# Kernel optimization log

Hardware: AMD Instinct MI355X
Metric: run time of the kernel (lower is better)

Reference implementation:

```python
import jax, jax.numpy as jnp
import numpy as np

BATCH, SEQ, HIDDEN = 2, 4096, 4096
HEADS, HEAD_DIM, BLOCK = 32, 128, 256
LAYER_IDX, N_LAYERS = 1, 32
EPS = 1e-5


def setup_inputs() -> dict:
    key = jax.random.key(0)
    ks = jax.random.split(key, 5)
    s = 0.02
    return {
        "hidden_states": jax.random.normal(ks[0], (BATCH, SEQ, HIDDEN), jnp.float32),
        "qkv_w": jax.random.normal(ks[1], (3 * HEADS * HEAD_DIM, HIDDEN), jnp.float32) * s,
        "out_w": jax.random.normal(ks[2], (HIDDEN, HEADS * HEAD_DIM), jnp.float32) * s,
        "gate_w": jax.random.normal(ks[3], (HEADS * HEAD_DIM, HIDDEN), jnp.float32) * s,
        "norm_w": jnp.ones((HEADS * HEAD_DIM,), jnp.float32),
    }


def _decays():
    # slope_rate: (h,1,1)
    base = 1.0 / 2.0 ** (8.0 / HEADS)
    exponent = jnp.arange(HEADS, dtype=jnp.float32) + 1.0
    factor = 1.0 - LAYER_IDX / (N_LAYERS - 1 + 1e-5) + 1e-5
    slope = (base ** exponent * factor)[:, None, None]
    r = jnp.arange(BLOCK, dtype=jnp.float32) + 1.0
    q_decay = jnp.exp(-slope * r[:, None])                 # (h, block, 1)
    k_decay = jnp.exp(-slope * (BLOCK - r)[:, None])       # (h, block, 1)
    diff = r[:, None] - r[None, :]                         # (block, block): i - j
    diag = slope[None] * diff[None, None]                  # (1, h, block, block)
    diag = jnp.where(diag >= 0, -diag, -jnp.inf)
    diag_decay = jnp.exp(diag)                             # causal intra-block decay
    block_decay = jnp.exp(-slope * BLOCK)                  # (h,1,1)
    return q_decay, k_decay, diag_decay, block_decay


def reference(hidden_states, qkv_w, out_w, gate_w, norm_w):
    b, s, _ = hidden_states.shape
    h, d, bs = HEADS, HEAD_DIM, BLOCK
    nb = s // bs
    q_decay, k_decay, diag_decay, block_decay = _decays()

    # qkv projection + silu, split per-head into q,k,v
    qkv = jax.nn.silu(hidden_states @ qkv_w.T)             # (b,s,3hd)
    qkv = qkv.reshape(b, s, h, 3, d)
    q = jnp.moveaxis(qkv[:, :, :, 0], 2, 1)                # (b,h,s,d)
    k = jnp.moveaxis(qkv[:, :, :, 1], 2, 1)
    v = jnp.moveaxis(qkv[:, :, :, 2], 2, 1)

    # split sequence into blocks, scan leading axis = block index
    def to_blocks(x):
        return jnp.moveaxis(x.reshape(b, h, nb, bs, d), 2, 0)  # (nb,b,h,bs,d)

    qb, kb, vb = to_blocks(q), to_blocks(k), to_blocks(v)

    def step(kv, blk):
        cq, ck, cv = blk
        # intra-block quadratic attention with causal decay
        scores = jnp.einsum('bhnd,bhmd->bhnm', cq, ck) * diag_decay
        intra = jnp.einsum('bhnm,bhmd->bhnd', scores, cv)
        # inter-block via decayed recurrent state kv: (b,h,d,d)
        inter = jnp.einsum('bhnd,bhde->bhne', cq * q_decay, kv)
        kv_next = kv * block_decay + jnp.einsum('bhnd,bhne->bhde', ck * k_decay, cv)
        return kv_next, intra + inter

    kv0 = jnp.zeros((b, h, d, d), hidden_states.dtype)
    _, out_blocks = jax.lax.scan(step, kv0, (qb, kb, vb))  # (nb,b,h,bs,d)

    attn = jnp.moveaxis(out_blocks, 0, 2)                  # (b,h,nb,bs,d)
    attn = attn.reshape(b, h, s, d).transpose(0, 2, 1, 3).reshape(b, s, h * d)

    # RMSNorm (fp32 accumulation, as MixtralRMSNorm)
    xf = attn.astype(jnp.float32)
    xf = xf * jax.lax.rsqrt(jnp.mean(xf * xf, axis=-1, keepdims=True) + EPS)
    normed = norm_w * xf.astype(attn.dtype)

    gate = jax.nn.sigmoid(hidden_states @ gate_w.T)
    return (gate * normed) @ out_w.T
```

## Files before the change

kernel.cpp:

```cpp
#include <hip/hip_runtime.h>

typedef unsigned short u16;
typedef __attribute__((ext_vector_type(4))) float f32x4;
typedef __attribute__((ext_vector_type(8))) __bf16 bf16x8;

#define SEQ   4096
#define HID   4096
#define HID3  12288

__device__ __forceinline__ float bf2f(u16 u){
  union { unsigned int i; float f; } v; v.i = ((unsigned int)u) << 16; return v.f;
}
__device__ __forceinline__ u16 f2bf(float f){
  union { float f; unsigned int i; } v; v.f = f;
  unsigned int r = (v.i + 0x7FFFu + ((v.i >> 16) & 1u)) >> 16;
  return (u16)r;
}
__device__ __forceinline__ float slope_of(int h){
  const float factor = 1.0f - 1.0f/(31.0f + 1e-5f) + 1e-5f;
  return exp2f(-0.25f * (float)(h + 1)) * factor;
}
__device__ __forceinline__ bf16x8 ld_bf8(const u16* p){
  return __builtin_bit_cast(bf16x8, *(const uint4*)p);
}
__device__ __forceinline__ void gload_lds16(const u16* g, u16* l){
  __builtin_amdgcn_global_load_lds((const __attribute__((address_space(1))) void*)g,
                                   (__attribute__((address_space(3))) void*)l, 16, 0, 0);
}

__global__ __launch_bounds__(256) void cvt_kernel(const float* __restrict__ in,
                                                  u16* __restrict__ out, long n){
  long i = ((long)blockIdx.x * 256 + threadIdx.x) * 4;
  long stride = (long)gridDim.x * 1024;
  for (; i < n; i += stride){
    float4 v = *(const float4*)(in + i);
    ushort4 o;
    o.x = f2bf(v.x); o.y = f2bf(v.y); o.z = f2bf(v.z); o.w = f2bf(v.w);
    *(ushort4*)(out + i) = o;
  }
}

template<int EPI>
__global__ __launch_bounds__(512) void gemm256(
    const u16* __restrict__ A, const u16* __restrict__ B, void* __restrict__ C,
    const u16* __restrict__ Aux, int M, int N, int K)
{
  __shared__ u16 ring[5][16384];
  const int t = threadIdx.x;
  const int w = t >> 6, l = t & 63, lr = l & 15, lk = l >> 4;
  const int mw = w >> 2, nw = w & 3;
  const int nbn = N >> 8;
  int nwg = gridDim.x;
  int bid = blockIdx.x;
  int bswz = (bid & 7) * (nwg >> 3) + (bid >> 3);
  int bm = bswz / nbn, bn = bswz % nbn;
  const u16* Abase = A + (long)(bm * 256) * K;
  const u16* Bbase = B + (long)(bn * 256) * K;
  const int NT = K >> 6;

  int sr[2], sku[2];
#pragma unroll
  for (int i = 0; i < 2; ++i){
    int dr = i * 64 + (t >> 3);
    int ul = (t & 7) ^ (dr & 7);
    sr[i]  = 2 * dr + (ul >> 2);
    sku[i] = ul & 3;
  }
  int offA[8], offB[4];
#pragma unroll
  for (int fn = 0; fn < 8; ++fn){
    int row = mw * 128 + fn * 16 + lr;
    offA[fn] = (row >> 1) * 64 + (((((row & 1) << 2) + lk) ^ ((row >> 1) & 7)) << 3);
  }
#pragma unroll
  for (int fe = 0; fe < 4; ++fe){
    int row = nw * 64 + fe * 16 + lr;
    offB[fe] = (row >> 1) * 64 + (((((row & 1) << 2) + lk) ^ ((row >> 1) & 7)) << 3);
  }

  auto stageA = [&](int kt, int c, int slot, int i){
    gload_lds16(Abase + (long)sr[i] * K + kt * 64 + c * 32 + sku[i] * 8,
                &ring[slot][i * 4096 + w * 512]);
  };
  auto stageB = [&](int kt, int c, int slot, int i){
    gload_lds16(Bbase + (long)sr[i] * K + kt * 64 + c * 32 + sku[i] * 8,
                &ring[slot][8192 + i * 4096 + w * 512]);
  };

  f32x4 acc[8][4] = {};

  stageA(0,0,0,0); stageA(0,0,0,1); stageB(0,0,0,0); stageB(0,0,0,1);
  stageA(0,1,1,0); stageA(0,1,1,1); stageB(0,1,1,0); stageB(0,1,1,1);
  if (1 < NT){ stageA(1,0,2,0); stageA(1,0,2,1); stageB(1,0,2,0); stageB(1,0,2,1); }
  asm volatile("s_waitcnt vmcnt(4)" ::: "memory");
  __builtin_amdgcn_s_barrier();

  int sa = 0;
  for (int p = 0; p < NT; ++p){
    int sb = sa + 1; if (sb >= 5) sb -= 5;
    int sx = sa + 3; if (sx >= 5) sx -= 5;
    int sy = sa + 4; if (sy >= 5) sy -= 5;
    const u16* Aa = &ring[sa][0];
    const u16* Ab = &ring[sb][0];
    const u16* Ba = &ring[sa][8192];
    const u16* Bb = &ring[sb][8192];
    bf16x8 bh[4][2], af[4][2][2];
#pragma unroll
    for (int q = 0; q < 4; ++q){
      if (q == 0){
#pragma unroll
        for (int fe = 0; fe < 4; ++fe){
          bh[fe][0] = ld_bf8(Ba + offB[fe]);
          bh[fe][1] = ld_bf8(Bb + offB[fe]);
        }
#pragma unroll
        for (int fnl = 0; fnl < 2; ++fnl){
          af[0][fnl][0] = ld_bf8(Aa + offA[fnl]);
          af[0][fnl][1] = ld_bf8(Ab + offA[fnl]);
        }
#pragma unroll
        for (int fnl = 0; fnl < 2; ++fnl){
          af[1][fnl][0] = ld_bf8(Aa + offA[2 + fnl]);
          af[1][fnl][1] = ld_bf8(Ab + offA[2 + fnl]);
        }
        if (p + 1 < NT){ stageA(p+1, 1, sx, 0); stageA(p+1, 1, sx, 1); }
      } else if (q == 1){
#pragma unroll
        for (int fnl = 0; fnl < 2; ++fnl){
          af[2][fnl][0] = ld_bf8(Aa + offA[4 + fnl]);
          af[2][fnl][1] = ld_bf8(Ab + offA[4 + fnl]);
        }
        if (p + 1 < NT){ stageB(p+1, 1, sx, 0); stageB(p+1, 1, sx, 1); }
      } else if (q == 2){
#pragma unroll
        for (int fnl = 0; fnl < 2; ++fnl){
          af[3][fnl][0] = ld_bf8(Aa + offA[6 + fnl]);
          af[3][fnl][1] = ld_bf8(Ab + offA[6 + fnl]);
        }
        if (p + 2 < NT){ stageA(p+2, 0, sy, 0); stageA(p+2, 0, sy, 1); }
      } else {
        if (p + 2 < NT){ stageB(p+2, 0, sy, 0); stageB(p+2, 0, sy, 1); }
      }
      if (q < 3) asm volatile("s_waitcnt lgkmcnt(4)" ::: "memory");
      else       asm volatile("s_waitcnt lgkmcnt(0)" ::: "memory");
      __builtin_amdgcn_sched_barrier(0);
      __builtin_amdgcn_s_setprio(1);
#pragma unroll
      for (int fnl = 0; fnl < 2; ++fnl)
#pragma unroll
        for (int fe = 0; fe < 4; ++fe){
          acc[q*2+fnl][fe] = __builtin_amdgcn_mfma_f32_16x16x32_bf16(af[q][fnl][0], bh[fe][0], acc[q*2+fnl][fe], 0, 0, 0);
          acc[q*2+fnl][fe] = __builtin_amdgcn_mfma_f32_16x16x32_bf16(af[q][fnl][1], bh[fe][1], acc[q*2+fnl][fe], 0, 0, 0);
        }
      __builtin_amdgcn_s_setprio(0);
    }
    if (p + 2 < NT) asm volatile("s_waitcnt vmcnt(4)" ::: "memory");
    else            asm volatile("s_waitcnt vmcnt(0)" ::: "memory");
    __builtin_amdgcn_s_barrier();
    sa += 2; if (sa >= 5) sa -= 5;
  }

  long crow = (long)bm * 256 + mw * 128 + lk * 4;
  long ccol = (long)bn * 256 + nw * 64 + lr;
#pragma unroll
  for (int fn = 0; fn < 8; ++fn)
#pragma unroll
    for (int fe = 0; fe < 4; ++fe)
#pragma unroll
      for (int reg = 0; reg < 4; ++reg){
        long row = crow + fn * 16 + reg;
        long col = ccol + fe * 16;
        float x = acc[fn][fe][reg];
        if (EPI == 0){
          ((u16*)C)[row * N + col] = f2bf(x / (1.0f + __expf(-x)));
        } else if (EPI == 1){
          float g = 1.0f / (1.0f + __expf(-x));
          ((u16*)C)[row * N + col] = f2bf(g * bf2f(Aux[row * N + col]));
        } else {
          ((float*)C)[row * N + col] = x;
        }
      }
}

__global__ __launch_bounds__(256) void attn_contrib(
    const u16* __restrict__ qkv, float* __restrict__ ct)
{
  __shared__ u16 kb[256 * 128];
  __shared__ u16 vb[256 * 128];
  __shared__ float kdec[256];
  int wg = blockIdx.x;
  int bh = wg >> 4, blk = wg & 15;
  int b = bh >> 5, h = bh & 31;
  int t = threadIdx.x;
  float slope = slope_of(h);
  kdec[t] = __expf(-slope * (float)(255 - t));
  const u16* kg = qkv + ((long)(b * SEQ + blk * 256)) * HID3 + h * 384 + 128;
  const u16* vg = kg + 128;
#pragma unroll
  for (int i = 0; i < 16; ++i){
    int chunk = t + i * 256;
    int row = chunk >> 4, c8 = (chunk & 15) << 3;
    *(uint4*)&kb[row * 128 + c8] = *(const uint4*)&kg[(long)row * HID3 + c8];
    *(uint4*)&vb[row * 128 + c8] = *(const uint4*)&vg[(long)row * HID3 + c8];
  }
  __syncthreads();
  int e0 = (t >> 4) << 3, d0 = (t & 15) << 3;
  float acc[8][8];
#pragma unroll
  for (int i = 0; i < 8; ++i)
#pragma unroll
    for (int j = 0; j < 8; ++j) acc[i][j] = 0.f;
  for (int n = 0; n < 256; ++n){
    float kd = kdec[n];
    uint4 vv = *(const uint4*)&vb[n * 128 + e0];
    uint4 kk = *(const uint4*)&kb[n * 128 + d0];
    const u16* vs = (const u16*)&vv;
    const u16* ks = (const u16*)&kk;
    float ve[8], kf[8];
#pragma unroll
    for (int x = 0; x < 8; ++x){ ve[x] = bf2f(vs[x]); kf[x] = bf2f(ks[x]) * kd; }
#pragma unroll
    for (int i = 0; i < 8; ++i)
#pragma unroll
      for (int j = 0; j < 8; ++j) acc[i][j] += ve[i] * kf[j];
  }
  float* out = ct + (long)wg * 16384;
#pragma unroll
  for (int i = 0; i < 8; ++i){
    *(float4*)&out[(e0 + i) * 128 + d0]     = make_float4(acc[i][0], acc[i][1], acc[i][2], acc[i][3]);
    *(float4*)&out[(e0 + i) * 128 + d0 + 4] = make_float4(acc[i][4], acc[i][5], acc[i][6], acc[i][7]);
  }
}

__global__ __launch_bounds__(256) void attn_scan(const float* __restrict__ ct,
                                                 u16* __restrict__ stTb)
{
  int g = blockIdx.x;
  int bh = g >> 2, sl = g & 3;
  int t = threadIdx.x;
  float bdec = __expf(-slope_of(bh & 31) * 256.0f);
  float cur[16];
#pragma unroll
  for (int i = 0; i < 16; ++i) cur[i] = 0.f;
  const float* base = ct + (long)bh * 16 * 16384 + sl * 4096;
  u16* ob = stTb + (long)bh * 16 * 16384 + sl * 4096;
  for (int blkI = 0; blkI < 16; ++blkI){
    const float* p = base + (long)blkI * 16384;
    u16* o = ob + (long)blkI * 16384;
#pragma unroll
    for (int i = 0; i < 16; ++i){
      o[t + i * 256] = f2bf(cur[i]);
      cur[i] = cur[i] * bdec + p[t + i * 256];
    }
  }
}

__global__ __launch_bounds__(512) void attn_mfma(
    const u16* __restrict__ qkv, const u16* __restrict__ stTb, u16* __restrict__ attn)
{
  __shared__ u16 Ks[256 * 130];
  __shared__ u16 VTs[128 * 258];
  __shared__ u16 Ps[4][64 * 34];
  int wg = blockIdx.x;
  int bh = wg >> 4, blk = wg & 15;
  int b = bh >> 5, h = bh & 31;
  int t = threadIdx.x;
  int w = t >> 6, l = t & 63, lr = l & 15, lk = l >> 4;
  int r = w >> 1, c = w & 1;
  float slope = slope_of(h);
  const u16* qg = qkv + ((long)(b * SEQ + blk * 256)) * HID3 + h * 384;
  const u16* kg = qg + 128;
  const u16* vg = qg + 256;

#pragma unroll
  for (int i = 0; i < 8; ++i){
    int chunk = t + i * 512;
    int row = chunk >> 4, c8 = (chunk & 15) << 3;
    *(uint4*)&Ks[row * 130 + c8] = *(const uint4*)&kg[(long)row * HID3 + c8];
    uint4 vv = *(const uint4*)&vg[(long)row * HID3 + c8];
    const u16* vs = (const u16*)&vv;
#pragma unroll
    for (int x = 0; x < 8; ++x) VTs[(c8 + x) * 258 + row] = vs[x];
  }
  bf16x8 qa[4][4];
#pragma unroll
  for (int fn = 0; fn < 4; ++fn)
#pragma unroll
    for (int kc = 0; kc < 4; ++kc)
      qa[fn][kc] = ld_bf8(&qg[(long)(r * 64 + fn * 16 + lr) * HID3 + kc * 32 + lk * 8]);
  f32x4 acc[4][4] = {};
  __syncthreads();

  int mtmax = 2 * r + 1;
  for (int mt = 0; mt < 8; ++mt){
    if (mt <= mtmax){
      f32x4 S[4] = {};
      int mrow = mt * 32 + c * 16 + lr;
      bf16x8 kb[4];
#pragma unroll
      for (int kc = 0; kc < 4; ++kc)
        kb[kc] = ld_bf8(&Ks[mrow * 130 + kc * 32 + lk * 8]);
#pragma unroll
      for (int fn = 0; fn < 4; ++fn)
#pragma unroll
        for (int kc = 0; kc < 4; ++kc)
          S[fn] = __builtin_amdgcn_mfma_f32_16x16x32_bf16(qa[fn][kc], kb[kc], S[fn], 0, 0, 0);
      int m = mt * 32 + c * 16 + lr;
#pragma unroll
      for (int fn = 0; fn < 4; ++fn)
#pragma unroll
        for (int reg = 0; reg < 4; ++reg){
          int n = r * 64 + fn * 16 + lk * 4 + reg;
          float dv = (n >= m) ? __expf(-slope * (float)(n - m)) : 0.f;
          Ps[r][(fn * 16 + lk * 4 + reg) * 34 + c * 16 + lr] = f2bf(S[fn][reg] * dv);
        }
    }
    __syncthreads();
    if (mt <= mtmax){
      bf16x8 pa[4], vb[4];
#pragma unroll
      for (int fn = 0; fn < 4; ++fn)
        pa[fn] = ld_bf8(&Ps[r][(fn * 16 + lr) * 34 + lk * 8]);
#pragma unroll
      for (int fe = 0; fe < 4; ++fe)
        vb[fe] = ld_bf8(&VTs[(c * 64 + fe * 16 + lr) * 258 + mt * 32 + lk * 8]);
#pragma unroll
      for (int fn = 0; fn < 4; ++fn)
#pragma unroll
        for (int fe = 0; fe < 4; ++fe)
          acc[fn][fe] = __builtin_amdgcn_mfma_f32_16x16x32_bf16(pa[fn], vb[fe], acc[fn][fe], 0, 0, 0);
    }
    __syncthreads();
  }

#pragma unroll
  for (int fn = 0; fn < 4; ++fn){
    int n = r * 64 + fn * 16 + lr;
    float qd = __expf(-slope * (float)(n + 1));
#pragma unroll
    for (int kc = 0; kc < 4; ++kc){
      union { bf16x8 v; u16 u[8]; } uu; uu.v = qa[fn][kc];
#pragma unroll
      for (int x = 0; x < 8; ++x) uu.u[x] = f2bf(bf2f(uu.u[x]) * qd);
      qa[fn][kc] = uu.v;
    }
  }
  const u16* sg = stTb + (long)(bh * 16 + blk) * 16384;
#pragma unroll
  for (int kc = 0; kc < 4; ++kc){
    bf16x8 sb2[4];
#pragma unroll
    for (int fe = 0; fe < 4; ++fe)
      sb2[fe] = ld_bf8(&sg[(c * 64 + fe * 16 + lr) * 128 + kc * 32 + lk * 8]);
#pragma unroll
    for (int fn = 0; fn < 4; ++fn)
#pragma unroll
      for (int fe = 0; fe < 4; ++fe)
        acc[fn][fe] = __builtin_amdgcn_mfma_f32_16x16x32_bf16(qa[fn][kc], sb2[fe], acc[fn][fe], 0, 0, 0);
  }

  u16* arow = attn + ((long)(b * SEQ + blk * 256)) * HID + h * 128;
#pragma unroll
  for (int fn = 0; fn < 4; ++fn)
#pragma unroll
    for (int fe = 0; fe < 4; ++fe)
#pragma unroll
      for (int reg = 0; reg < 4; ++reg){
        int n = r * 64 + fn * 16 + lk * 4 + reg;
        int col = c * 64 + fe * 16 + lr;
        arow[(long)n * HID + col] = f2bf(acc[fn][fe][reg]);
      }
}

__global__ __launch_bounds__(256) void rmsnorm_ip(u16* __restrict__ attn,
                                                  const float* __restrict__ nw)
{
  __shared__ float wsum[4];
  int row = blockIdx.x, t = threadIdx.x;
  u16* p = attn + (long)row * HID;
  uint4 v0 = *(const uint4*)&p[t * 8];
  uint4 v1 = *(const uint4*)&p[t * 8 + 2048];
  const u16* a0 = (const u16*)&v0;
  const u16* a1 = (const u16*)&v1;
  float f0[8], f1[8];
  float ss = 0.f;
#pragma unroll
  for (int x = 0; x < 8; ++x){
    f0[x] = bf2f(a0[x]); f1[x] = bf2f(a1[x]);
    ss += f0[x] * f0[x] + f1[x] * f1[x];
  }
#pragma unroll
  for (int off = 32; off > 0; off >>= 1) ss += __shfl_down(ss, off);
  if ((t & 63) == 0) wsum[t >> 6] = ss;
  __syncthreads();
  float rs = rsqrtf((wsum[0] + wsum[1] + wsum[2] + wsum[3]) * (1.0f / 4096.0f) + 1e-5f);
  alignas(16) u16 o0[8], o1[8];
#pragma unroll
  for (int x = 0; x < 8; ++x){
    o0[x] = f2bf(f0[x] * rs * nw[t * 8 + x]);
    o1[x] = f2bf(f1[x] * rs * nw[t * 8 + 2048 + x]);
  }
  *(uint4*)&p[t * 8]        = *(const uint4*)&o0[0];
  *(uint4*)&p[t * 8 + 2048] = *(const uint4*)&o1[0];
}

extern "C" void kernel_launch(void* const* d_in, const int* in_sizes, int n_in,
                              void* d_out, int out_size, void* d_ws, size_t ws_size,
                              hipStream_t stream)
{
  const float* hidden = (const float*)d_in[0];
  const float* qkv_w  = (const float*)d_in[1];
  const float* out_w  = (const float*)d_in[2];
  const float* gate_w = (const float*)d_in[3];
  const float* norm_w = (const float*)d_in[4];
  char* ws = (char*)d_ws;
  const long SZ_X  = 67108864L;
  const long SZ_WQ = 100663296L;
  const long SZ_WG = 33554432L;
  const long SZ_WO = 33554432L;
  const long SZ_QA = 201326592L;
  const long SZ_AT = 67108864L;
  u16* Xb   = (u16*)(ws);
  u16* Wq   = (u16*)(ws + SZ_X);
  u16* Wg   = (u16*)(ws + SZ_X + SZ_WQ);
  u16* Wo   = (u16*)(ws + SZ_X + SZ_WQ + SZ_WG);
  u16* qact = (u16*)(ws + SZ_X + SZ_WQ + SZ_WG + SZ_WO);
  u16* attn = (u16*)(ws + SZ_X + SZ_WQ + SZ_WG + SZ_WO + SZ_QA);
  float* st   = (float*)Wq;
  u16*   stTb = (u16*)(ws + SZ_X + 67108864L);
  u16* gated = qact;
  if (ws_size < (size_t)(SZ_X + SZ_WQ + SZ_WG + SZ_WO + SZ_QA + SZ_AT)) return;

  cvt_kernel<<<1024, 256, 0, stream>>>(hidden, Xb, 33554432L);
  cvt_kernel<<<1024, 256, 0, stream>>>(qkv_w,  Wq, 50331648L);
  cvt_kernel<<<1024, 256, 0, stream>>>(gate_w, Wg, 16777216L);
  cvt_kernel<<<1024, 256, 0, stream>>>(out_w,  Wo, 16777216L);

  gemm256<0><<<32 * 48, 512, 0, stream>>>(Xb, Wq, (void*)qact, nullptr, 8192, 12288, 4096);

  attn_contrib<<<1024, 256, 0, stream>>>(qact, st);
  attn_scan<<<256, 256, 0, stream>>>(st, stTb);
  attn_mfma<<<1024, 512, 0, stream>>>(qact, stTb, attn);
  rmsnorm_ip<<<8192, 256, 0, stream>>>(attn, norm_w);

  gemm256<1><<<32 * 16, 512, 0, stream>>>(Xb, Wg, (void*)gated, attn, 8192, 4096, 4096);
  gemm256<2><<<32 * 16, 512, 0, stream>>>(gated, Wo, d_out, nullptr, 8192, 4096, 4096);
}
```

Baseline: 1.699 ms.

## Use MFMA for per-block KV contribution and fuse the four fp32-to-bf16 conversions

attn_contrib now stages K (pre-multiplied by its decay) and V transposed in padded shared memory and computes the 128x128 V^T·K block product with bf16 MFMA instructions instead of scalar FMA loops. The four conversion launches are merged into one kernel over a contiguous destination buffer, relying on the workspace segments being adjacent. Rounding K·decay back to bf16 before the product adds a small precision loss. The transposed, strided LDS writes may cause bank conflicts.

```diff
diff --git a/kernel.cpp b/kernel.cpp
--- a/kernel.cpp
+++ b/kernel.cpp
@@ -28,15 +28,28 @@
                                    (__attribute__((address_space(3))) void*)l, 16, 0, 0);
 }
 
-__global__ __launch_bounds__(256) void cvt_kernel(const float* __restrict__ in,
-                                                  u16* __restrict__ out, long n){
+#define CVT_B0 33554432L
+#define CVT_B1 83886080L
+#define CVT_B2 100663296L
+#define CVT_B3 117440512L
+__global__ __launch_bounds__(256) void cvt4_kernel(const float* __restrict__ s0,
+                                                   const float* __restrict__ s1,
+                                                   const float* __restrict__ s2,
+                                                   const float* __restrict__ s3,
+                                                   u16* __restrict__ dst){
   long i = ((long)blockIdx.x * 256 + threadIdx.x) * 4;
   long stride = (long)gridDim.x * 1024;
-  for (; i < n; i += stride){
-    float4 v = *(const float4*)(in + i);
+  for (; i < CVT_B3; i += stride){
+    const float* src;
+    long off;
+    if (i < CVT_B0){ src = s0; off = i; }
+    else if (i < CVT_B1){ src = s1; off = i - CVT_B0; }
+    else if (i < CVT_B2){ src = s2; off = i - CVT_B1; }
+    else { src = s3; off = i - CVT_B2; }
+    float4 v = *(const float4*)(src + off);
     ushort4 o;
     o.x = f2bf(v.x); o.y = f2bf(v.y); o.z = f2bf(v.z); o.w = f2bf(v.w);
-    *(ushort4*)(out + i) = o;
+    *(ushort4*)(dst + i) = o;
   }
 }
 
@@ -185,51 +198,57 @@
 __global__ __launch_bounds__(256) void attn_contrib(
     const u16* __restrict__ qkv, float* __restrict__ ct)
 {
-  __shared__ u16 kb[256 * 128];
-  __shared__ u16 vb[256 * 128];
-  __shared__ float kdec[256];
+  __shared__ u16 VT[128 * 258];
+  __shared__ u16 KT[128 * 258];
   int wg = blockIdx.x;
   int bh = wg >> 4, blk = wg & 15;
   int b = bh >> 5, h = bh & 31;
   int t = threadIdx.x;
   float slope = slope_of(h);
-  kdec[t] = __expf(-slope * (float)(255 - t));
   const u16* kg = qkv + ((long)(b * SEQ + blk * 256)) * HID3 + h * 384 + 128;
   const u16* vg = kg + 128;
 #pragma unroll
   for (int i = 0; i < 16; ++i){
     int chunk = t + i * 256;
     int row = chunk >> 4, c8 = (chunk & 15) << 3;
-    *(uint4*)&kb[row * 128 + c8] = *(const uint4*)&kg[(long)row * HID3 + c8];
-    *(uint4*)&vb[row * 128 + c8] = *(const uint4*)&vg[(long)row * HID3 + c8];
+    float kd = __expf(-slope * (float)(255 - row));
+    uint4 kk = *(const uint4*)&kg[(long)row * HID3 + c8];
+    uint4 vv = *(const uint4*)&vg[(long)row * HID3 + c8];
+    const u16* ks = (const u16*)&kk;
+    const u16* vs = (const u16*)&vv;
+#pragma unroll
+    for (int x = 0; x < 8; ++x){
+      KT[(c8 + x) * 258 + row] = f2bf(bf2f(ks[x]) * kd);
+      VT[(c8 + x) * 258 + row] = vs[x];
+    }
   }
   __syncthreads();
-  int e0 = (t >> 4) << 3, d0 = (t & 15) << 3;
-  float acc[8][8];
-#pragma unroll
-  for (int i = 0; i < 8; ++i)
-#pragma unroll
-    for (int j = 0; j < 8; ++j) acc[i][j] = 0.f;
-  for (int n = 0; n < 256; ++n){
-    float kd = kdec[n];
-    uint4 vv = *(const uint4*)&vb[n * 128 + e0];
-    uint4 kk = *(const uint4*)&kb[n * 128 + d0];
-    const u16* vs = (const u16*)&vv;
-    const u16* ks = (const u16*)&kk;
-    float ve[8], kf[8];
-#pragma unroll
-    for (int x = 0; x < 8; ++x){ ve[x] = bf2f(vs[x]); kf[x] = bf2f(ks[x]) * kd; }
-#pragma unroll
-    for (int i = 0; i < 8; ++i)
-#pragma unroll
-      for (int j = 0; j < 8; ++j) acc[i][j] += ve[i] * kf[j];
+  int w = t >> 6, l = t & 63, lr = l & 15, lk = l >> 4;
+  int we = (w >> 1) * 64, wd = (w & 1) * 64;
+  f32x4 acc[4][4] = {};
+  for (int nc = 0; nc < 8; ++nc){
+    bf16x8 va[4], kb[4];
+#pragma unroll
+    for (int f = 0; f < 4; ++f) va[f] = ld_bf8(&VT[(we + f * 16 + lr) * 258 + nc * 32 + lk * 8]);
+#pragma unroll
+    for (int f = 0; f < 4; ++f) kb[f] = ld_bf8(&KT[(wd + f * 16 + lr) * 258 + nc * 32 + lk * 8]);
+#pragma unroll
+    for (int fe = 0; fe < 4; ++fe)
+#pragma unroll
+      for (int fd = 0; fd < 4; ++fd)
+        acc[fe][fd] = __builtin_amdgcn_mfma_f32_16x16x32_bf16(va[fe], kb[fd], acc[fe][fd], 0, 0, 0);
   }
   float* out = ct + (long)wg * 16384;
 #pragma unroll
-  for (int i = 0; i < 8; ++i){
-    *(float4*)&out[(e0 + i) * 128 + d0]     = make_float4(acc[i][0], acc[i][1], acc[i][2], acc[i][3]);
-    *(float4*)&out[(e0 + i) * 128 + d0 + 4] = make_float4(acc[i][4], acc[i][5], acc[i][6], acc[i][7]);
-  }
+  for (int fe = 0; fe < 4; ++fe)
+#pragma unroll
+    for (int fd = 0; fd < 4; ++fd)
+#pragma unroll
+      for (int reg = 0; reg < 4; ++reg){
+        int e = we + fe * 16 + lk * 4 + reg;
+        int d = wd + fd * 16 + lr;
+        out[e * 128 + d] = acc[fe][fd][reg];
+      }
 }
 
 __global__ __launch_bounds__(256) void attn_scan(const float* __restrict__ ct,
@@ -431,10 +450,7 @@
   u16* gated = qact;
   if (ws_size < (size_t)(SZ_X + SZ_WQ + SZ_WG + SZ_WO + SZ_QA + SZ_AT)) return;
 
-  cvt_kernel<<<1024, 256, 0, stream>>>(hidden, Xb, 33554432L);
-  cvt_kernel<<<1024, 256, 0, stream>>>(qkv_w,  Wq, 50331648L);
-  cvt_kernel<<<1024, 256, 0, stream>>>(gate_w, Wg, 16777216L);
-  cvt_kernel<<<1024, 256, 0, stream>>>(out_w,  Wo, 16777216L);
+  cvt4_kernel<<<2048, 256, 0, stream>>>(hidden, qkv_w, gate_w, out_w, Xb);
 
   gemm256<0><<<32 * 48, 512, 0, stream>>>(Xb, Wq, (void*)qact, nullptr, 8192, 12288, 4096);
 
```

After: 1.585 ms. 6.7% less time.
